# Kernel optimization log

Measured on AMD Instinct MI355X. Metric: run time of the kernel, lower is better.

Reference implementation:

```python
import jax, jax.numpy as jnp
import numpy as np

EMBED = 768
HEADS = 12
HEAD_DIM = EMBED // HEADS
B, S = 1, 4096


def setup_inputs() -> dict:
    key = jax.random.key(0)
    ks = jax.random.split(key, 8)
    values = jax.random.normal(ks[0], (B, S, EMBED), dtype=jnp.float32)
    keys_in = jax.random.normal(ks[1], (B, S, EMBED), dtype=jnp.float32)
    queries = jax.random.normal(ks[2], (B, S, EMBED), dtype=jnp.float32)
    # causal mask: 1.0 where attention is disallowed (gets * -1e9)
    mask = jnp.triu(jnp.ones((S, S), dtype=jnp.float32), k=1)[None, None, :, :]
    sc = 1.0 / np.sqrt(EMBED)
    W_q = jax.random.normal(ks[3], (EMBED, EMBED), dtype=jnp.float32) * sc
    W_k = jax.random.normal(ks[4], (EMBED, EMBED), dtype=jnp.float32) * sc
    W_v = jax.random.normal(ks[5], (EMBED, EMBED), dtype=jnp.float32) * sc
    W_o = jax.random.normal(ks[6], (EMBED, EMBED), dtype=jnp.float32) * sc
    b_o = jnp.zeros((EMBED,), dtype=jnp.float32)
    return {"values": values, "keys": keys_in, "queries": queries, "mask": mask,
            "W_q": W_q, "W_k": W_k, "W_v": W_v, "W_o": W_o, "b_o": b_o}


def reference(values, keys, queries, mask, W_q, W_k, W_v, W_o, b_o):
    N, S_, _ = queries.shape
    # linear projections (Dense, no bias)
    q = queries @ W_q  # [N, S, E]
    k = keys @ W_k
    v = values @ W_v
    # split heads -> [N, H, S, Dh]
    def split(x):
        return x.reshape(N, S_, HEADS, HEAD_DIM).transpose(0, 2, 1, 3)
    q, k, v = split(q), split(k), split(v)
    scores = jnp.einsum('nhqd,nhkd->nhqk', q, k) / jnp.sqrt(
        jnp.asarray(HEAD_DIM, dtype=q.dtype))
    scores = scores + mask * (-1e9)
    attn = jax.nn.softmax(scores, axis=-1)
    out = jnp.einsum('nhqk,nhkd->nhqd', attn, v)  # [N, H, S, Dh]
    out = out.transpose(0, 2, 1, 3).reshape(N, S_, EMBED)
    return out @ W_o + b_o
```

## Files before the change

### kernel.cpp

```cpp
#include <hip/hip_runtime.h>

#define S_LEN 4096
#define EMB   768
#define NH    12
#define DH    64

typedef __attribute__((ext_vector_type(8))) short bf16x8;
typedef __attribute__((ext_vector_type(4))) float f32x4;

__device__ __forceinline__ unsigned short f2bf(float f) {
    union { float f; unsigned u; } v; v.f = f;
    unsigned r = v.u + 0x7fffu + ((v.u >> 16) & 1u);
    return (unsigned short)(r >> 16);
}
__device__ __forceinline__ float bf2f(unsigned short u) {
    union { unsigned u; float f; } v; v.u = (unsigned)u << 16; return v.f;
}
__device__ __forceinline__ unsigned pk2(float lo, float hi) {
    unsigned r;
    asm("v_cvt_pk_bf16_f32 %0, %1, %2" : "=v"(r) : "v"(lo), "v"(hi));
    return r;
}
__device__ __forceinline__ float fexp2(float x) {
    float r;
    asm("v_exp_f32 %0, %1" : "=v"(r) : "v"(x));
    return r;
}
__device__ __forceinline__ f32x4 mfma16(bf16x8 a, bf16x8 b, f32x4 c) {
    return __builtin_amdgcn_mfma_f32_16x16x32_bf16(a, b, c, 0, 0, 0);
}
__device__ __forceinline__ void async16(unsigned short* lds, const unsigned short* g) {
    __builtin_amdgcn_global_load_lds(
        (const __attribute__((address_space(1))) unsigned int*)(const void*)g,
        (__attribute__((address_space(3))) unsigned int*)(void*)lds, 16, 0, 0);
}

#define QSCALE 0.180336884f

__global__ __launch_bounds__(256) void prep(const float* __restrict__ Wq, const float* __restrict__ Wk,
                     const float* __restrict__ Wv, const float* __restrict__ Wo,
                     const float* __restrict__ q_in, const float* __restrict__ k_in,
                     const float* __restrict__ v_in,
                     unsigned short* __restrict__ WT, unsigned short* __restrict__ conv) {
    int bx = blockIdx.x, t = threadIdx.x;
    if (bx < 576) {
        __shared__ float tile[64][65];
        int z = bx / 144, rem = bx % 144;
        int k0 = (rem / 12) * 64, n0 = (rem % 12) * 64;
        const float* W = (z == 0) ? Wq : (z == 1) ? Wk : (z == 2) ? Wv : Wo;
        unsigned short* out = WT + (size_t)z * EMB * EMB;
        int row = t >> 2, c = (t & 3) * 16;
        const float4* src = (const float4*)(W + (size_t)(k0 + row) * EMB + n0 + c);
#pragma unroll
        for (int i = 0; i < 4; i++) {
            float4 v = src[i];
            tile[row][c + i * 4 + 0] = v.x; tile[row][c + i * 4 + 1] = v.y;
            tile[row][c + i * 4 + 2] = v.z; tile[row][c + i * 4 + 3] = v.w;
        }
        __syncthreads();
        unsigned short tmp[16] __attribute__((aligned(16)));
#pragma unroll
        for (int i = 0; i < 16; i++) tmp[i] = f2bf(tile[c + i][row]);
        int4* dst = (int4*)(out + (size_t)(n0 + row) * EMB + k0 + c);
        dst[0] = *(int4*)&tmp[0];
        dst[1] = *(int4*)&tmp[8];
    } else {
        size_t e8 = ((size_t)(bx - 576) * 256 + t) * 8;
        int z = (int)(e8 / 3145728);
        size_t off = e8 - (size_t)z * 3145728;
        const float* src = (z == 0) ? q_in : (z == 1) ? k_in : v_in;
        float4 a = *(const float4*)(src + off);
        float4 b = *(const float4*)(src + off + 4);
        unsigned r[4];
        r[0] = pk2(a.x, a.y); r[1] = pk2(a.z, a.w);
        r[2] = pk2(b.x, b.y); r[3] = pk2(b.z, b.w);
        *(int4*)(conv + e8) = *(int4*)r;
    }
}

__global__ __launch_bounds__(256) void gemm_qkv(const unsigned short* __restrict__ conv,
                                                const unsigned short* __restrict__ WT,
                                                unsigned short* __restrict__ Qh,
                                                unsigned short* __restrict__ Kh,
                                                unsigned short* __restrict__ Vt) {
    __shared__ unsigned short As[64 * 32];
    __shared__ unsigned short Bs[128 * 32];
    int m0 = blockIdx.x * 64;
    int z = blockIdx.y / 6, n0 = (blockIdx.y % 6) * 128;
    const unsigned short* A  = conv + (size_t)z * 3145728;
    const unsigned short* Bt = WT   + (size_t)z * 589824;
    int t = threadIdx.x, lane = t & 63, wv = t >> 6, quad = lane >> 4, l16 = lane & 15;
    int wn = wv;
    int cfr = (quad ^ ((l16 >> 1) & 3)) * 8;

    int rA = t >> 2, gcA = (t & 3) ^ ((rA >> 1) & 3);
    const unsigned short* pa = A + (size_t)(m0 + rA) * EMB + gcA * 8;
    const unsigned short* pb[2];
#pragma unroll
    for (int a2 = 0; a2 < 2; a2++) {
        int s1 = a2 * 256 + t, rB = s1 >> 2, gcB = (s1 & 3) ^ ((rB >> 1) & 3);
        pb[a2] = Bt + (size_t)(n0 + rB) * EMB + gcB * 8;
    }
    f32x4 acc[4][2] = {};

    for (int k0 = 0; k0 < EMB; k0 += 32) {
        async16(&As[t * 8], pa + k0);
#pragma unroll
        for (int a2 = 0; a2 < 2; a2++)
            async16(&Bs[(a2 * 256 + t) * 8], pb[a2] + k0);
        __syncthreads();
        bf16x8 fa[4], fb[2];
#pragma unroll
        for (int mi = 0; mi < 4; mi++)
            fa[mi] = *(bf16x8*)&As[(mi * 16 + l16) * 32 + cfr];
#pragma unroll
        for (int ni = 0; ni < 2; ni++)
            fb[ni] = *(bf16x8*)&Bs[(wn * 32 + ni * 16 + l16) * 32 + cfr];
#pragma unroll
        for (int mi = 0; mi < 4; mi++)
#pragma unroll
            for (int ni = 0; ni < 2; ni++)
                acc[mi][ni] = mfma16(fa[mi], fb[ni], acc[mi][ni]);
        __syncthreads();
    }

    if (z == 2) {
#pragma unroll
        for (int mi = 0; mi < 4; mi++)
#pragma unroll
            for (int ni = 0; ni < 2; ni++) {
                int m = m0 + mi * 16 + quad * 4;
                int n = n0 + wn * 32 + ni * 16 + l16;
                uint2 val;
                val.x = pk2(acc[mi][ni][0], acc[mi][ni][1]);
                val.y = pk2(acc[mi][ni][2], acc[mi][ni][3]);
                *(uint2*)&Vt[(size_t)(((n >> 6) << 6) + (n & 63)) * S_LEN + m] = val;
            }
    } else {
        unsigned short* dst = z ? Kh : Qh;
        float sc = z ? 1.0f : QSCALE;
#pragma unroll
        for (int mi = 0; mi < 4; mi++)
#pragma unroll
            for (int ni = 0; ni < 2; ni++)
#pragma unroll
                for (int r = 0; r < 4; r++) {
                    int m = m0 + mi * 16 + quad * 4 + r;
                    int n = n0 + wn * 32 + ni * 16 + l16;
                    dst[((size_t)(n >> 6) * S_LEN + m) * 64 + (n & 63)] = f2bf(acc[mi][ni][r] * sc);
                }
    }
}

__global__ __launch_bounds__(256) void attn_kernel(const unsigned short* __restrict__ Qh,
                                                   const unsigned short* __restrict__ Kh,
                                                   const unsigned short* __restrict__ Vt,
                                                   unsigned short* __restrict__ Opart,
                                                   float* __restrict__ Lpart) {
    __shared__ unsigned short Kls[2][4096];
    __shared__ unsigned short Vls[2][4096];
    __shared__ unsigned short Pls[4 * 32 * 72];

    int p = blockIdx.x, h = blockIdx.y;
    int qb2 = 0, pre = 0;
    while (pre + (qb2 >> 2) + 1 <= p) { pre += (qb2 >> 2) + 1; qb2++; }
    int sp = p - pre;
    int part = h * 144 + p;
    int ntile = 2 * qb2 + 2;
    int jb = sp * 8, je = min(jb + 8, ntile);
    int q0 = qb2 << 7;

    int t = threadIdx.x, w = t >> 6, lane = t & 63, quad = lane >> 4, l16 = lane & 15;
    int rb = w * 32;
    int c0 = (quad ^ (l16 & 7)) * 8, c1 = (((quad + 4) ^ (l16 & 7))) * 8;

    const unsigned short* kb_ = Kh + (size_t)h * S_LEN * DH;
    const unsigned short* vb_ = Vt + (size_t)h * S_LEN * DH;

    bf16x8 aQ[2][2];
#pragma unroll
    for (int rg = 0; rg < 2; rg++)
#pragma unroll
        for (int kh = 0; kh < 2; kh++)
            aQ[rg][kh] = *(const bf16x8*)(Qh + ((size_t)h * S_LEN + q0 + rb + rg * 16 + l16) * 64 + kh * 32 + quad * 8);

    const unsigned short* pk_[2];
    const unsigned short* pv_[2];
    int ldso[2];
#pragma unroll
    for (int a2 = 0; a2 < 2; a2++) {
        int s1 = a2 * 256 + t, r = s1 >> 3, gc = (s1 & 7) ^ (r & 7);
        pk_[a2] = kb_ + (size_t)(jb * 64 + r) * 64 + gc * 8;
        pv_[a2] = vb_ + (size_t)r * S_LEN + jb * 64 + gc * 8;
        ldso[a2] = s1 * 8;
    }

    f32x4 o[4][2] = {};
    float lsum[2] = {0.f, 0.f};
    unsigned short* pwave = &Pls[w * 32 * 72];

#pragma unroll 1
    for (int jt = jb; jt < je; jt++) {
        int buf = (jt - jb) & 1;
        if (jt == jb) {
#pragma unroll
            for (int a2 = 0; a2 < 2; a2++) {
                async16(&Kls[0][ldso[a2]], pk_[a2]); pk_[a2] += 4096;
                async16(&Vls[0][ldso[a2]], pv_[a2]); pv_[a2] += 64;
            }
        }
        __syncthreads();
        if (jt + 1 < je) {
#pragma unroll
            for (int a2 = 0; a2 < 2; a2++) {
                async16(&Kls[buf ^ 1][ldso[a2]], pk_[a2]); pk_[a2] += 4096;
                async16(&Vls[buf ^ 1][ldso[a2]], pv_[a2]); pv_[a2] += 64;
            }
        }
        bool active = !(jt == 2 * qb2 + 1 && w < 2);
        if (active) {
            f32x4 s[2][4];
#pragma unroll
            for (int nt = 0; nt < 4; nt++) {
                int row = nt * 16 + l16;
                bf16x8 k0f = *(bf16x8*)&Kls[buf][row * 64 + c0];
                bf16x8 k1f = *(bf16x8*)&Kls[buf][row * 64 + c1];
#pragma unroll
                for (int rg = 0; rg < 2; rg++) {
                    f32x4 zz = {};
                    zz = mfma16(k0f, aQ[rg][0], zz);
                    zz = mfma16(k1f, aQ[rg][1], zz);
                    s[rg][nt] = zz;
                }
            }
            if (jt >= 2 * qb2) {
                int dlt = (jt - 2 * qb2) * 64;
#pragma unroll
                for (int rg = 0; rg < 2; rg++) {
                    int qrel = rb + rg * 16 + l16 - dlt;
#pragma unroll
                    for (int nt = 0; nt < 4; nt++)
#pragma unroll
                        for (int r = 0; r < 4; r++)
                            if (nt * 16 + quad * 4 + r > qrel) s[rg][nt][r] = -1e9f;
                }
            }
#pragma unroll
            for (int rg = 0; rg < 2; rg++)
#pragma unroll
                for (int nt = 0; nt < 4; nt++) {
                    float p0 = fexp2(s[rg][nt][0]);
                    float p1 = fexp2(s[rg][nt][1]);
                    float p2 = fexp2(s[rg][nt][2]);
                    float p3 = fexp2(s[rg][nt][3]);
                    lsum[rg] += (p0 + p1) + (p2 + p3);
                    uint2 val;
                    val.x = pk2(p0, p1);
                    val.y = pk2(p2, p3);
                    *(uint2*)&pwave[(rg * 16 + l16) * 72 + nt * 16 + quad * 4] = val;
                }
            asm volatile("s_waitcnt lgkmcnt(0)" ::: "memory");
            bf16x8 bP[2][2];
#pragma unroll
            for (int ntq = 0; ntq < 2; ntq++) {
                bP[ntq][0] = *(bf16x8*)&pwave[(ntq * 16 + l16) * 72 + quad * 8];
                bP[ntq][1] = *(bf16x8*)&pwave[(ntq * 16 + l16) * 72 + 32 + quad * 8];
            }
#pragma unroll
            for (int mt = 0; mt < 4; mt++) {
                int row = mt * 16 + l16;
                bf16x8 v0f = *(bf16x8*)&Vls[buf][row * 64 + c0];
                bf16x8 v1f = *(bf16x8*)&Vls[buf][row * 64 + c1];
#pragma unroll
                for (int ntq = 0; ntq < 2; ntq++) {
                    o[mt][ntq] = mfma16(v0f, bP[ntq][0], o[mt][ntq]);
                    o[mt][ntq] = mfma16(v1f, bP[ntq][1], o[mt][ntq]);
                }
            }
        }
    }

    unsigned short* op = Opart + (size_t)part * 8192;
#pragma unroll
    for (int mt = 0; mt < 4; mt++)
#pragma unroll
        for (int ntq = 0; ntq < 2; ntq++) {
            uint2 val;
            val.x = pk2(o[mt][ntq][0], o[mt][ntq][1]);
            val.y = pk2(o[mt][ntq][2], o[mt][ntq][3]);
            int q = rb + ntq * 16 + l16;
            int d = mt * 16 + quad * 4;
            *(uint2*)&op[q * 64 + d] = val;
        }
    float* lp = Lpart + (size_t)part * 128;
#pragma unroll
    for (int rg = 0; rg < 2; rg++) {
        float v = lsum[rg];
        v += __shfl_xor(v, 16); v += __shfl_xor(v, 32);
        if (quad == 0) lp[rb + rg * 16 + l16] = v;
    }
}

__global__ __launch_bounds__(256) void merge(const unsigned short* __restrict__ Opart,
                                             const float* __restrict__ Lpart,
                                             unsigned short* __restrict__ O) {
    int qb2 = blockIdx.x, h = blockIdx.y;
    int a = qb2 >> 2, b = qb2 & 3;
    int pre = qb2 + 2 * a * (a - 1) + a * b;
    int cnt = a + 1;
    int pbase = h * 144 + pre;
    int t = threadIdx.x, row = t >> 1, ch = (t & 1) * 32;

    float acc[32] = {};
    float ls = 0.f;
    const unsigned short* src = Opart + (size_t)pbase * 8192 + row * 64 + ch;
    for (int p2 = 0; p2 < cnt; p2++) {
        ls += Lpart[(size_t)(pbase + p2) * 128 + row];
        const int4* s4 = (const int4*)(src + (size_t)p2 * 8192);
#pragma unroll
        for (int i = 0; i < 4; i++) {
            int4 x = s4[i];
            const unsigned short* xs = (const unsigned short*)&x;
#pragma unroll
            for (int j = 0; j < 8; j++) acc[i * 8 + j] += bf2f(xs[j]);
        }
    }
    float inv = 1.0f / ls;
    unsigned outp[16];
#pragma unroll
    for (int i = 0; i < 16; i++) outp[i] = pk2(acc[2 * i] * inv, acc[2 * i + 1] * inv);
    int4* dst = (int4*)(O + (size_t)(qb2 * 128 + row) * EMB + h * 64 + ch);
#pragma unroll
    for (int i = 0; i < 4; i++) dst[i] = *(int4*)&outp[i * 4];
}

__global__ __launch_bounds__(256) void gemm_out(const unsigned short* __restrict__ O,
                                                const unsigned short* __restrict__ WT,
                                                const float* __restrict__ bias,
                                                float* __restrict__ out) {
    __shared__ unsigned short As[64 * 32];
    __shared__ unsigned short Bs[64 * 32];
    int m0 = blockIdx.x * 64, n0 = blockIdx.y * 64;
    const unsigned short* Bt = WT + (size_t)3 * 589824;
    int t = threadIdx.x, lane = t & 63, wv = t >> 6, quad = lane >> 4, l16 = lane & 15;
    int wm = wv >> 1, wn = wv & 1;
    int cfr = (quad ^ ((l16 >> 1) & 3)) * 8;

    int rA = t >> 2, gcA = (t & 3) ^ ((rA >> 1) & 3);
    const unsigned short* pa = O  + (size_t)(m0 + rA) * EMB + gcA * 8;
    const unsigned short* pb = Bt + (size_t)(n0 + rA) * EMB + gcA * 8;
    f32x4 acc[2][2] = {};

    for (int k0 = 0; k0 < EMB; k0 += 32) {
        async16(&As[t * 8], pa + k0);
        async16(&Bs[t * 8], pb + k0);
        __syncthreads();
        bf16x8 fa[2], fb[2];
#pragma unroll
        for (int mi = 0; mi < 2; mi++)
            fa[mi] = *(bf16x8*)&As[(wm * 32 + mi * 16 + l16) * 32 + cfr];
#pragma unroll
        for (int ni = 0; ni < 2; ni++)
            fb[ni] = *(bf16x8*)&Bs[(wn * 32 + ni * 16 + l16) * 32 + cfr];
#pragma unroll
        for (int mi = 0; mi < 2; mi++)
#pragma unroll
            for (int ni = 0; ni < 2; ni++)
                acc[mi][ni] = mfma16(fa[mi], fb[ni], acc[mi][ni]);
        __syncthreads();
    }

    float bv[2];
#pragma unroll
    for (int ni = 0; ni < 2; ni++) bv[ni] = bias[n0 + wn * 32 + ni * 16 + l16];
#pragma unroll
    for (int mi = 0; mi < 2; mi++)
#pragma unroll
        for (int ni = 0; ni < 2; ni++)
#pragma unroll
            for (int r = 0; r < 4; r++) {
                int m = m0 + wm * 32 + mi * 16 + quad * 4 + r;
                int n = n0 + wn * 32 + ni * 16 + l16;
                out[(size_t)m * EMB + n] = acc[mi][ni][r] + bv[ni];
            }
}

extern "C" void kernel_launch(void* const* d_in, const int* in_sizes, int n_in,
                              void* d_out, int out_size, void* d_ws, size_t ws_size,
                              hipStream_t stream) {
    const float* values  = (const float*)d_in[0];
    const float* keys    = (const float*)d_in[1];
    const float* queries = (const float*)d_in[2];
    const float* Wq = (const float*)d_in[4];
    const float* Wk = (const float*)d_in[5];
    const float* Wv = (const float*)d_in[6];
    const float* Wo = (const float*)d_in[7];
    const float* bo = (const float*)d_in[8];

    char* ws = (char*)d_ws;
    unsigned short* WT = (unsigned short*)ws;
    unsigned short* Qh = (unsigned short*)(ws + 4718592);
    unsigned short* Kh = (unsigned short*)(ws + 11010048);
    unsigned short* Vt = (unsigned short*)(ws + 17301504);
    unsigned short* O  = (unsigned short*)(ws + 23592960);
    unsigned short* conv = (unsigned short*)(ws + 29884416);
    unsigned short* Op   = (unsigned short*)(ws + 29884416);
    float*          Lp   = (float*)(ws + 29884416 + 28311552);
    float* out = (float*)d_out;

    prep<<<dim3(5184), 256, 0, stream>>>(Wq, Wk, Wv, Wo, queries, keys, values, WT, conv);
    gemm_qkv<<<dim3(64, 18), 256, 0, stream>>>(conv, WT, Qh, Kh, Vt);
    attn_kernel<<<dim3(144, 12), 256, 0, stream>>>(Qh, Kh, Vt, Op, Lp);
    merge<<<dim3(32, 12), 256, 0, stream>>>(Op, Lp, O);
    gemm_out<<<dim3(64, 12), 256, 0, stream>>>(O, WT, bo, out);
}
```

Before: 245.0 us.

## Single-buffer K/V tiles and shrink P scratch to raise attention occupancy

Replaces the double-buffered K/V shared-memory tiles with one buffer and a barrier at the end of each iteration. The per-wave P scratch shrinks by processing the two 16-row query groups one after the other, so each P tile is written and read back before the next. Adds a launch bound that asks for 5 blocks per CU. Together these cut LDS use and register pressure so more blocks can be resident, trading away the overlap of the next tile's load with the current tile's compute and adding an extra barrier per tile.

Measured after the change: 371.4 us. 1.52x slower.

```diff
diff --git a/kernel.cpp b/kernel.cpp
--- a/kernel.cpp
+++ b/kernel.cpp
@@ -152,14 +152,14 @@
     }
 }
 
-__global__ __launch_bounds__(256) void attn_kernel(const unsigned short* __restrict__ Qh,
-                                                   const unsigned short* __restrict__ Kh,
-                                                   const unsigned short* __restrict__ Vt,
-                                                   unsigned short* __restrict__ Opart,
-                                                   float* __restrict__ Lpart) {
-    __shared__ unsigned short Kls[2][4096];
-    __shared__ unsigned short Vls[2][4096];
-    __shared__ unsigned short Pls[4 * 32 * 72];
+__global__ __launch_bounds__(256, 5) void attn_kernel(const unsigned short* __restrict__ Qh,
+                                                      const unsigned short* __restrict__ Kh,
+                                                      const unsigned short* __restrict__ Vt,
+                                                      unsigned short* __restrict__ Opart,
+                                                      float* __restrict__ Lpart) {
+    __shared__ unsigned short Kls[4096];
+    __shared__ unsigned short Vls[4096];
+    __shared__ unsigned short Pls[4 * 16 * 72];
 
     int p = blockIdx.x, h = blockIdx.y;
     int qb2 = 0, pre = 0;
@@ -197,34 +197,24 @@
 
     f32x4 o[4][2] = {};
     float lsum[2] = {0.f, 0.f};
-    unsigned short* pwave = &Pls[w * 32 * 72];
+    unsigned short* pwave = &Pls[w * 16 * 72];
 
 #pragma unroll 1
     for (int jt = jb; jt < je; jt++) {
-        int buf = (jt - jb) & 1;
-        if (jt == jb) {
-#pragma unroll
-            for (int a2 = 0; a2 < 2; a2++) {
-                async16(&Kls[0][ldso[a2]], pk_[a2]); pk_[a2] += 4096;
-                async16(&Vls[0][ldso[a2]], pv_[a2]); pv_[a2] += 64;
-            }
+#pragma unroll
+        for (int a2 = 0; a2 < 2; a2++) {
+            async16(&Kls[ldso[a2]], pk_[a2]); pk_[a2] += 4096;
+            async16(&Vls[ldso[a2]], pv_[a2]); pv_[a2] += 64;
         }
         __syncthreads();
-        if (jt + 1 < je) {
-#pragma unroll
-            for (int a2 = 0; a2 < 2; a2++) {
-                async16(&Kls[buf ^ 1][ldso[a2]], pk_[a2]); pk_[a2] += 4096;
-                async16(&Vls[buf ^ 1][ldso[a2]], pv_[a2]); pv_[a2] += 64;
-            }
-        }
         bool active = !(jt == 2 * qb2 + 1 && w < 2);
         if (active) {
             f32x4 s[2][4];
 #pragma unroll
             for (int nt = 0; nt < 4; nt++) {
                 int row = nt * 16 + l16;
-                bf16x8 k0f = *(bf16x8*)&Kls[buf][row * 64 + c0];
-                bf16x8 k1f = *(bf16x8*)&Kls[buf][row * 64 + c1];
+                bf16x8 k0f = *(bf16x8*)&Kls[row * 64 + c0];
+                bf16x8 k1f = *(bf16x8*)&Kls[row * 64 + c1];
 #pragma unroll
                 for (int rg = 0; rg < 2; rg++) {
                     f32x4 zz = {};
@@ -246,7 +236,7 @@
                 }
             }
 #pragma unroll
-            for (int rg = 0; rg < 2; rg++)
+            for (int rg = 0; rg < 2; rg++) {
 #pragma unroll
                 for (int nt = 0; nt < 4; nt++) {
                     float p0 = fexp2(s[rg][nt][0]);
@@ -254,30 +244,24 @@
                     float p2 = fexp2(s[rg][nt][2]);
                     float p3 = fexp2(s[rg][nt][3]);
                     lsum[rg] += (p0 + p1) + (p2 + p3);
-                    uint2 val;
-                    val.x = pk2(p0, p1);
-                    val.y = pk2(p2, p3);
-                    *(uint2*)&pwave[(rg * 16 + l16) * 72 + nt * 16 + quad * 4] = val;
+                    unsigned short* pw = &pwave[l16 * 72 + nt * 16 + quad * 4];
+                    *(unsigned*)&pw[0] = pk2(p0, p1);
+                    *(unsigned*)&pw[2] = pk2(p2, p3);
                 }
-            asm volatile("s_waitcnt lgkmcnt(0)" ::: "memory");
-            bf16x8 bP[2][2];
-#pragma unroll
-            for (int ntq = 0; ntq < 2; ntq++) {
-                bP[ntq][0] = *(bf16x8*)&pwave[(ntq * 16 + l16) * 72 + quad * 8];
-                bP[ntq][1] = *(bf16x8*)&pwave[(ntq * 16 + l16) * 72 + 32 + quad * 8];
-            }
-#pragma unroll
-            for (int mt = 0; mt < 4; mt++) {
-                int row = mt * 16 + l16;
-                bf16x8 v0f = *(bf16x8*)&Vls[buf][row * 64 + c0];
-                bf16x8 v1f = *(bf16x8*)&Vls[buf][row * 64 + c1];
-#pragma unroll
-                for (int ntq = 0; ntq < 2; ntq++) {
-                    o[mt][ntq] = mfma16(v0f, bP[ntq][0], o[mt][ntq]);
-                    o[mt][ntq] = mfma16(v1f, bP[ntq][1], o[mt][ntq]);
+                asm volatile("s_waitcnt lgkmcnt(0)" ::: "memory");
+                bf16x8 bP0 = *(bf16x8*)&pwave[l16 * 72 + quad * 8];
+                bf16x8 bP1 = *(bf16x8*)&pwave[l16 * 72 + 32 + quad * 8];
+#pragma unroll
+                for (int mt = 0; mt < 4; mt++) {
+                    int row = mt * 16 + l16;
+                    bf16x8 v0f = *(bf16x8*)&Vls[row * 64 + c0];
+                    bf16x8 v1f = *(bf16x8*)&Vls[row * 64 + c1];
+                    o[mt][rg] = mfma16(v0f, bP0, o[mt][rg]);
+                    o[mt][rg] = mfma16(v1f, bP1, o[mt][rg]);
                 }
             }
         }
+        __syncthreads();
     }
 
     unsigned short* op = Opart + (size_t)part * 8192;
```
